# Optimization experiments

Hardware: AMD Instinct MI355X
Metric: run time of the kernel (lower is better)

The kernel has to match this reference:

```python
import jax, jax.numpy as jnp
import numpy as np

MAX_ITERS = 20
TOL = 1e-6
STEP = 1.0
EPS = 1e-7
CLIP = 1e-7


def _normalize(x, axis=-1):
    n = jnp.linalg.norm(x, axis=axis, keepdims=True)
    return x / jnp.maximum(n, 1e-12)


def _safe_acos(x):
    return jnp.arccos(jnp.clip(x, -1.0 + CLIP, 1.0 - CLIP))


def setup_inputs() -> dict:
    key = jax.random.key(0)
    NC, K, N, D = 1000, 8, 32, 128
    X_groups = jax.random.normal(key, (NC, K, N, D), dtype=jnp.float32)
    return {"X_groups": X_groups}


def reference(X_groups):
    # X_groups: (NC, K, N, D)
    NC, K, N, D = X_groups.shape
    X = X_groups.reshape(NC * K, N, D)
    Xn = _normalize(X)                      # (G, N, D) unit vectors
    mu = _normalize(jnp.mean(Xn, axis=1))   # (G, D) init mean

    done = jnp.array(False)
    for _ in range(MAX_ITERS):
        dots = jnp.einsum('gd,gnd->gn', mu, Xn)             # (G, N)
        theta = _safe_acos(dots)
        sin_t = jnp.maximum(jnp.sin(theta), EPS)
        diff = Xn - dots[..., None] * mu[:, None, :]        # (G, N, D)
        log_vecs = (theta / sin_t)[..., None] * diff        # log map
        v = jnp.mean(log_vecs, axis=1)                      # (G, D)
        v_norm = jnp.maximum(jnp.linalg.norm(v, axis=-1, keepdims=True), EPS)
        done = done | (jnp.max(v_norm) < TOL)               # global convergence (as in torch .item() check)
        v_step = STEP * v
        vs_norm = jnp.maximum(jnp.linalg.norm(v_step, axis=-1, keepdims=True), EPS)
        mu_new = jnp.cos(vs_norm) * mu + jnp.sin(vs_norm) * (v_step / vs_norm)  # exp map
        mu_new = _normalize(mu_new)
        mu = jnp.where(done, mu, mu_new)

    # calc_cluster_distance: features (G, N, D) @ means (G, D)
    sims = jnp.einsum('gnd,gd->gn', Xn, mu)
    sims = jnp.clip(sims, -1 + CLIP, 1 - CLIP)
    loss = jnp.mean(jnp.sum(jnp.arccos(sims) ** 2, axis=-1))
    return loss
```

## Files before the change

### kernel.cpp

```cpp
#include <hip/hip_runtime.h>
#include <stdint.h>

#define MAX_ITERS 20
#define EPSV 1e-7f
#define CLIPV 1e-7f
#define PI_F 3.14159265358979f
#define PIO2_F 1.57079632679490f

typedef __attribute__((ext_vector_type(8))) short short8;
typedef __attribute__((ext_vector_type(4))) float f4;

__device__ __forceinline__ f4 mfma_bf16(short8 a, short8 b, f4 c) {
    return __builtin_amdgcn_mfma_f32_16x16x32_bf16(a, b, c, 0, 0, 0);
}

__device__ __forceinline__ float rl(float v, int l) {
    return __int_as_float(__builtin_amdgcn_readlane(__float_as_int(v), l));
}

template <int CTRL>
__device__ __forceinline__ float dpp_add(float v) {
    int p = __builtin_amdgcn_update_dpp(0, __float_as_int(v), CTRL, 0xF, 0xF, true);
    return v + __int_as_float(p);
}
template <int CTRL>
__device__ __forceinline__ float dpp_mov(float v) {
    return __int_as_float(__builtin_amdgcn_update_dpp(0, __float_as_int(v), CTRL, 0xF, 0xF, true));
}

template <int PAT>
__device__ __forceinline__ float swz(float v) {
    return __int_as_float(__builtin_amdgcn_ds_swizzle(__float_as_int(v), PAT));
}

__device__ __forceinline__ float rowsum16(float v) {
    v = dpp_add<0xB1>(v);
    v = dpp_add<0x4E>(v);
    v = dpp_add<0x141>(v);
    v = dpp_add<0x140>(v);
    return v;
}

__device__ __forceinline__ float halfsum_rl(float v, bool hB) {
    v = rowsum16(v);
    float sA = rl(v, 0) + rl(v, 16);
    float sB = rl(v, 32) + rl(v, 48);
    return hB ? sB : sA;
}

__device__ __forceinline__ float halfsum_sw(float v) {
    v = rowsum16(v);
    return v + swz<0x401F>(v);
}

__device__ __forceinline__ float fast_acos(float x) {
    float a = fabsf(x);
    bool big = a > 0.5f;
    float z = big ? 0.5f * (1.0f - a) : x * x;
    float s = big ? sqrtf(z) : x;
    float p = fmaf(z, fmaf(z, fmaf(z, fmaf(z, 4.2163199048e-2f, 2.4181311049e-2f),
                                   4.5470025998e-2f), 7.4953002686e-2f),
                   1.6666752422e-1f);
    float r = fmaf(s * z, p, s);
    float big_val = (x < 0.0f) ? (PI_F - 2.0f * r) : (2.0f * r);
    return big ? big_val : (PIO2_F - r);
}

__device__ __forceinline__ void cvt_hilo(const float* v, short8& hi, short8& lo) {
#pragma unroll
    for (int i = 0; i < 8; ++i) {
        float x = v[i];
        uint32_t u = __float_as_uint(x);
        float hf = __uint_as_float(u & 0xFFFF0000u);
        float lf = x - hf;
        hi[i] = (short)(u >> 16);
        lo[i] = (short)(__float_as_uint(lf) >> 16);
    }
}

#define CHAIN8(cur, acc, B)                                          \
    acc = Grow2[B] * cur;                                            \
    cur = dpp_mov<0xB1>(cur);  acc = fmaf(Grow2[(B)^1],  cur, acc);  \
    cur = dpp_mov<0x4E>(cur);  acc = fmaf(Grow2[(B)^3],  cur, acc);  \
    cur = dpp_mov<0xB1>(cur);  acc = fmaf(Grow2[(B)^2],  cur, acc);  \
    cur = dpp_mov<0x128>(cur); acc = fmaf(Grow2[(B)^10], cur, acc);  \
    cur = dpp_mov<0xB1>(cur);  acc = fmaf(Grow2[(B)^11], cur, acc);  \
    cur = dpp_mov<0x4E>(cur);  acc = fmaf(Grow2[(B)^9],  cur, acc);  \
    cur = dpp_mov<0xB1>(cur);  acc = fmaf(Grow2[(B)^8],  cur, acc);

#define GLOAD_LDS16(srcp, ldsp)                                                   \
    __builtin_amdgcn_global_load_lds(                                             \
        (const __attribute__((address_space(1))) uint32_t*)(srcp),                \
        (__attribute__((address_space(3))) uint32_t*)(ldsp), 16, 0, 0)

#define WAIT_VM(N) do {                                        \
        asm volatile("s_waitcnt vmcnt(" #N ")" ::: "memory");  \
        __builtin_amdgcn_sched_barrier(0);                     \
    } while (0)

__device__ __forceinline__ int gidx(int row, int j) {
    return row * 32 + ((((j >> 2) ^ (row & 7)) << 2) | (j & 3));
}

__global__ void __launch_bounds__(128, 4) karcher(const float* __restrict__ X,
                                                  float* __restrict__ ws,
                                                  int n_groups) {
    __shared__ float lds[2][3072];
    __shared__ float sInv[2][64];
    __shared__ float sPart[4];

    const int lane = threadIdx.x & 63;
    const int wid  = threadIdx.x >> 6;
    const int g0   = blockIdx.x * 4 + wid * 2;
    if (g0 >= n_groups) return;

    const int col  = lane & 15;
    const int quad = lane >> 4;

    float* slot0 = lds[wid];
    float* slot1 = lds[wid] + 1024;
    float* slot2 = lds[wid] + 2048;

    const int rrl = lane >> 3;
    const int g2l = lane & 7;
    auto stage = [&](const float* Xg, int kq, float* slot) {
#pragma unroll
        for (int i = 0; i < 4; ++i) {
            int rr  = i * 8 + rrl;
            int g2s = g2l ^ (rr & 7);
            GLOAD_LDS16(Xg + rr * 128 + kq * 32 + g2s * 4, slot + i * 256);
        }
    };

    const int x0 = col & 7;
    const int b0 = col * 32;
    const int b1 = (col + 16) * 32;
    f4 a00 = {0.f, 0.f, 0.f, 0.f}, a01 = a00, a10 = a00, a11 = a00;
    auto gramq = [&](const float* st) {
        int s0 = ((quad * 2 + 0) ^ x0) * 4;
        int s1 = ((quad * 2 + 1) ^ x0) * 4;
        float r0[8], r1[8];
        *(float4*)(r0)     = *(const float4*)(st + b0 + s0);
        *(float4*)(r0 + 4) = *(const float4*)(st + b0 + s1);
        *(float4*)(r1)     = *(const float4*)(st + b1 + s0);
        *(float4*)(r1 + 4) = *(const float4*)(st + b1 + s1);
        short8 H0, L0, H1, L1;
        cvt_hilo(r0, H0, L0);
        cvt_hilo(r1, H1, L1);
        a00 = mfma_bf16(H0, H0, a00);
        a00 = mfma_bf16(H0, L0, a00);
        a00 = mfma_bf16(L0, H0, a00);
        a01 = mfma_bf16(H0, H1, a01);
        a01 = mfma_bf16(H0, L1, a01);
        a01 = mfma_bf16(L0, H1, a01);
        a10 = mfma_bf16(H1, H0, a10);
        a10 = mfma_bf16(H1, L0, a10);
        a10 = mfma_bf16(L1, H0, a10);
        a11 = mfma_bf16(H1, H1, a11);
        a11 = mfma_bf16(H1, L1, a11);
        a11 = mfma_bf16(L1, H1, a11);
    };
    auto writeG = [&](float* Gs) {
#pragma unroll
        for (int i = 0; i < 4; ++i) {
            int rw = quad * 4 + i;
            Gs[gidx(rw,      col)]      = a00[i];
            Gs[gidx(rw,      col + 16)] = a01[i];
            Gs[gidx(rw + 16, col)]      = a10[i];
            Gs[gidx(rw + 16, col + 16)] = a11[i];
        }
    };

    {
        const float* Xa = X + (size_t)g0 * 4096;
        const float* Xb = X + (size_t)(g0 + 1) * 4096;
        stage(Xa, 0, slot0);
        stage(Xa, 1, slot1);
        WAIT_VM(4);  gramq(slot0);  stage(Xa, 2, slot0);
        WAIT_VM(4);  gramq(slot1);  stage(Xa, 3, slot1);
        WAIT_VM(4);  gramq(slot0);  stage(Xb, 0, slot0);
        WAIT_VM(4);  gramq(slot1);
        writeG(slot2);
        a00 = {0.f, 0.f, 0.f, 0.f}; a01 = a00; a10 = a00; a11 = a00;
        stage(Xb, 1, slot1);
        WAIT_VM(4);  gramq(slot0);  stage(Xb, 2, slot0);
        WAIT_VM(4);  gramq(slot1);  stage(Xb, 3, slot1);
        WAIT_VM(4);  gramq(slot0);
        WAIT_VM(0);  gramq(slot1);
        writeG(slot0);
    }

    const int  half = lane >> 5;
    const bool hB   = half != 0;
    const int  r    = lane & 31;
    const float* Gh = hB ? slot0 : slot2;

    float inv = 1.0f / fmaxf(sqrtf(Gh[gidx(r, r)]), 1e-12f);
    sInv[wid][lane] = inv;
    const float* sI = sInv[wid] + half * 32;

    float Grow2[32];
#pragma unroll
    for (int gg = 0; gg < 32; ++gg) {
        int j = r ^ gg;
        Grow2[gg] = Gh[gidx(r, j)] * (inv * sI[j]);
    }

    float a = 1.0f / 32.0f;
    float ga;
    {
        float s0 = 0, s1 = 0, s2 = 0, s3 = 0;
#pragma unroll
        for (int gg = 0; gg < 8; ++gg) {
            s0 += Grow2[gg];
            s1 += Grow2[gg + 8];
            s2 += Grow2[gg + 16];
            s3 += Grow2[gg + 24];
        }
        ga = ((s0 + s1) + (s2 + s3)) * (1.0f / 32.0f);
        float n2   = halfsum_rl(a * ga, hB);
        float inv0 = 1.0f / fmaxf(sqrtf(n2), 1e-12f);
        a  *= inv0;
        ga *= inv0;
    }

    for (int it = 0; it < MAX_ITERS; ++it) {
        float x  = fminf(fmaxf(ga, -1.0f + CLIPV), 1.0f - CLIPV);
        float th = fast_acos(x);
        float st = fmaxf(sqrtf(fmaxf(1.0f - x * x, 0.0f)), EPSV);
        float w  = __fdividef(th, st);

        float w4  = swz<0x101F>(w);
        float w16 = swz<0x401F>(w);
        float w20 = swz<0x501F>(w);
        float C = halfsum_sw(w * ga);

        float c0 = w,  c1 = w4, c2 = w16, c3 = w20;
        float A0, A1, A2, A3;
        CHAIN8(c0, A0, 0)
        CHAIN8(c1, A1, 4)
        CHAIN8(c2, A2, 16)
        CHAIN8(c3, A3, 20)
        float gw = (A0 + A1) + (A2 + A3);

        float gb   = (gw - C * ga) * (1.0f / 32.0f);
        float beta = (w  - C * a ) * (1.0f / 32.0f);

        float vv = halfsum_rl(beta * gb, hB);
        float vs = fmaxf(sqrtf(fmaxf(vv, 0.0f)), EPSV);
        float cv = __cosf(vs);
        float sv = __fdividef(__sinf(vs), vs);
        a  = fmaf(sv, beta, cv * a);
        ga = fmaf(sv, gb, cv * ga);
        if (__all(vs < 1e-6f)) break;
    }

    float xf = fminf(fmaxf(ga, -1.0f + CLIPV), 1.0f - CLIPV);
    float t  = fast_acos(xf);
    float ls = halfsum_rl(t * t, hB);
    if (r == 0) sPart[wid * 2 + half] = ls;
    __syncthreads();
    if (threadIdx.x == 0)
        ws[blockIdx.x] = (sPart[0] + sPart[1]) + (sPart[2] + sPart[3]);
}

__global__ void __launch_bounds__(256) reduce_partials(const float* __restrict__ ws,
                                                       float* __restrict__ out,
                                                       int n, float scale) {
    __shared__ float sred[4];
    float s = 0.f;
    for (int i = threadIdx.x; i < n; i += 256) s += ws[i];
#pragma unroll
    for (int m = 32; m >= 1; m >>= 1) s += __shfl_xor(s, m, 64);
    const int lane = threadIdx.x & 63, wid = threadIdx.x >> 6;
    if (lane == 0) sred[wid] = s;
    __syncthreads();
    if (threadIdx.x == 0)
        out[0] = ((sred[0] + sred[1]) + (sred[2] + sred[3])) * scale;
}

extern "C" void kernel_launch(void* const* d_in, const int* in_sizes, int n_in,
                              void* d_out, int out_size, void* d_ws, size_t ws_size,
                              hipStream_t stream) {
    const float* X = (const float*)d_in[0];
    float* out = (float*)d_out;
    float* ws = (float*)d_ws;
    int n_groups = in_sizes[0] / (32 * 128);
    int blocks = (n_groups + 3) / 4;
    karcher<<<blocks, 128, 0, stream>>>(X, ws, n_groups);
    reduce_partials<<<1, 256, 0, stream>>>(ws, out, blocks, 1.0f / (float)n_groups);
}
```

Baseline: 213.9 us.

## Map one group per wavefront with finer-grained double-buffered staging

Each wavefront now handles a single group instead of two, and blocks grow to 256 threads with four waves. The Gram staging is restructured into eight smaller 16-column chunks, double-buffered in a 512-float slot per wave, with explicit LDS waits. The aim is more waves in flight to hide global load latency and a smaller per-wave LDS footprint. In exchange, half of each wave's lanes do duplicate work in the per-group iteration, since the two halves of the wave hold the same group, and the reductions now read lanes 0 and 16 only.

```diff
diff --git a/kernel.cpp b/kernel.cpp
--- a/kernel.cpp
+++ b/kernel.cpp
@@ -27,7 +27,6 @@
 __device__ __forceinline__ float dpp_mov(float v) {
     return __int_as_float(__builtin_amdgcn_update_dpp(0, __float_as_int(v), CTRL, 0xF, 0xF, true));
 }
-
 template <int PAT>
 __device__ __forceinline__ float swz(float v) {
     return __int_as_float(__builtin_amdgcn_ds_swizzle(__float_as_int(v), PAT));
@@ -41,16 +40,9 @@
     return v;
 }
 
-__device__ __forceinline__ float halfsum_rl(float v, bool hB) {
+__device__ __forceinline__ float wavesum32(float v) {
     v = rowsum16(v);
-    float sA = rl(v, 0) + rl(v, 16);
-    float sB = rl(v, 32) + rl(v, 48);
-    return hB ? sB : sA;
-}
-
-__device__ __forceinline__ float halfsum_sw(float v) {
-    v = rowsum16(v);
-    return v + swz<0x401F>(v);
+    return rl(v, 0) + rl(v, 16);
 }
 
 __device__ __forceinline__ float fast_acos(float x) {
@@ -97,113 +89,107 @@
         asm volatile("s_waitcnt vmcnt(" #N ")" ::: "memory");  \
         __builtin_amdgcn_sched_barrier(0);                     \
     } while (0)
+#define WAIT_LGKM0() do {                                      \
+        asm volatile("s_waitcnt lgkmcnt(0)" ::: "memory");     \
+        __builtin_amdgcn_sched_barrier(0);                     \
+    } while (0)
 
 __device__ __forceinline__ int gidx(int row, int j) {
     return row * 32 + ((((j >> 2) ^ (row & 7)) << 2) | (j & 3));
 }
 
-__global__ void __launch_bounds__(128, 4) karcher(const float* __restrict__ X,
+__global__ void __launch_bounds__(256, 8) karcher(const float* __restrict__ X,
                                                   float* __restrict__ ws,
                                                   int n_groups) {
-    __shared__ float lds[2][3072];
-    __shared__ float sInv[2][64];
+    __shared__ float lds[4][1024];
+    __shared__ float sInv[4][32];
     __shared__ float sPart[4];
 
     const int lane = threadIdx.x & 63;
     const int wid  = threadIdx.x >> 6;
-    const int g0   = blockIdx.x * 4 + wid * 2;
-    if (g0 >= n_groups) return;
+    const int g    = blockIdx.x * 4 + wid;
+    if (g >= n_groups) return;
 
     const int col  = lane & 15;
     const int quad = lane >> 4;
+    const float* Xg = X + (size_t)g * 4096;
 
     float* slot0 = lds[wid];
-    float* slot1 = lds[wid] + 1024;
-    float* slot2 = lds[wid] + 2048;
-
-    const int rrl = lane >> 3;
-    const int g2l = lane & 7;
-    auto stage = [&](const float* Xg, int kq, float* slot) {
-#pragma unroll
-        for (int i = 0; i < 4; ++i) {
-            int rr  = i * 8 + rrl;
-            int g2s = g2l ^ (rr & 7);
-            GLOAD_LDS16(Xg + rr * 128 + kq * 32 + g2s * 4, slot + i * 256);
+    float* slot1 = lds[wid] + 512;
+
+    const int rrl = lane >> 2;
+    const int gcl = lane & 3;
+    auto stage = [&](int t, float* slot) {
+#pragma unroll
+        for (int i = 0; i < 2; ++i) {
+            int rr = i * 16 + rrl;
+            GLOAD_LDS16(Xg + rr * 128 + t * 16 + gcl * 4, slot + i * 256);
         }
     };
 
-    const int x0 = col & 7;
-    const int b0 = col * 32;
-    const int b1 = (col + 16) * 32;
     f4 a00 = {0.f, 0.f, 0.f, 0.f}, a01 = a00, a10 = a00, a11 = a00;
-    auto gramq = [&](const float* st) {
-        int s0 = ((quad * 2 + 0) ^ x0) * 4;
-        int s1 = ((quad * 2 + 1) ^ x0) * 4;
-        float r0[8], r1[8];
-        *(float4*)(r0)     = *(const float4*)(st + b0 + s0);
-        *(float4*)(r0 + 4) = *(const float4*)(st + b0 + s1);
-        *(float4*)(r1)     = *(const float4*)(st + b1 + s0);
-        *(float4*)(r1 + 4) = *(const float4*)(st + b1 + s1);
-        short8 H0, L0, H1, L1;
-        cvt_hilo(r0, H0, L0);
-        cvt_hilo(r1, H1, L1);
-        a00 = mfma_bf16(H0, H0, a00);
-        a00 = mfma_bf16(H0, L0, a00);
-        a00 = mfma_bf16(L0, H0, a00);
-        a01 = mfma_bf16(H0, H1, a01);
-        a01 = mfma_bf16(H0, L1, a01);
-        a01 = mfma_bf16(L0, H1, a01);
-        a10 = mfma_bf16(H1, H0, a10);
-        a10 = mfma_bf16(H1, L0, a10);
-        a10 = mfma_bf16(L1, H0, a10);
-        a11 = mfma_bf16(H1, H1, a11);
-        a11 = mfma_bf16(H1, L1, a11);
-        a11 = mfma_bf16(L1, H1, a11);
-    };
-    auto writeG = [&](float* Gs) {
-#pragma unroll
-        for (int i = 0; i < 4; ++i) {
-            int rw = quad * 4 + i;
-            Gs[gidx(rw,      col)]      = a00[i];
-            Gs[gidx(rw,      col + 16)] = a01[i];
-            Gs[gidx(rw + 16, col)]      = a10[i];
-            Gs[gidx(rw + 16, col + 16)] = a11[i];
-        }
-    };
-
-    {
-        const float* Xa = X + (size_t)g0 * 4096;
-        const float* Xb = X + (size_t)(g0 + 1) * 4096;
-        stage(Xa, 0, slot0);
-        stage(Xa, 1, slot1);
-        WAIT_VM(4);  gramq(slot0);  stage(Xa, 2, slot0);
-        WAIT_VM(4);  gramq(slot1);  stage(Xa, 3, slot1);
-        WAIT_VM(4);  gramq(slot0);  stage(Xb, 0, slot0);
-        WAIT_VM(4);  gramq(slot1);
-        writeG(slot2);
-        a00 = {0.f, 0.f, 0.f, 0.f}; a01 = a00; a10 = a00; a11 = a00;
-        stage(Xb, 1, slot1);
-        WAIT_VM(4);  gramq(slot0);  stage(Xb, 2, slot0);
-        WAIT_VM(4);  gramq(slot1);  stage(Xb, 3, slot1);
-        WAIT_VM(4);  gramq(slot0);
-        WAIT_VM(0);  gramq(slot1);
-        writeG(slot0);
-    }
-
-    const int  half = lane >> 5;
-    const bool hB   = half != 0;
-    const int  r    = lane & 31;
-    const float* Gh = hB ? slot0 : slot2;
-
-    float inv = 1.0f / fmaxf(sqrtf(Gh[gidx(r, r)]), 1e-12f);
-    sInv[wid][lane] = inv;
-    const float* sI = sInv[wid] + half * 32;
+    float r0[8], r1[8];
+
+#define PHASE(T, WN)                                                        \
+    {                                                                       \
+        WAIT_VM(WN);                                                        \
+        const float* st = ((T) & 1) ? slot1 : slot0;                        \
+        *(float4*)(r0 + 4 * ((T) & 1)) =                                    \
+            *(const float4*)(st + col * 16 + quad * 4);                     \
+        *(float4*)(r1 + 4 * ((T) & 1)) =                                    \
+            *(const float4*)(st + (col + 16) * 16 + quad * 4);              \
+        WAIT_LGKM0();                                                       \
+        if ((T) + 2 < 8) stage((T) + 2, ((T) & 1) ? slot1 : slot0);         \
+        if ((T) & 1) {                                                      \
+            short8 H0, L0, H1, L1;                                          \
+            cvt_hilo(r0, H0, L0);                                           \
+            cvt_hilo(r1, H1, L1);                                           \
+            a00 = mfma_bf16(H0, H0, a00);                                   \
+            a00 = mfma_bf16(H0, L0, a00);                                   \
+            a00 = mfma_bf16(L0, H0, a00);                                   \
+            a01 = mfma_bf16(H0, H1, a01);                                   \
+            a01 = mfma_bf16(H0, L1, a01);                                   \
+            a01 = mfma_bf16(L0, H1, a01);                                   \
+            a10 = mfma_bf16(H1, H0, a10);                                   \
+            a10 = mfma_bf16(H1, L0, a10);                                   \
+            a10 = mfma_bf16(L1, H0, a10);                                   \
+            a11 = mfma_bf16(H1, H1, a11);                                   \
+            a11 = mfma_bf16(H1, L1, a11);                                   \
+            a11 = mfma_bf16(L1, H1, a11);                                   \
+        }                                                                   \
+    }
+
+    stage(0, slot0);
+    stage(1, slot1);
+    PHASE(0, 2)
+    PHASE(1, 2)
+    PHASE(2, 2)
+    PHASE(3, 2)
+    PHASE(4, 2)
+    PHASE(5, 2)
+    PHASE(6, 2)
+    PHASE(7, 0)
+#undef PHASE
+
+    float* Gw = lds[wid];
+#pragma unroll
+    for (int i = 0; i < 4; ++i) {
+        int rw = quad * 4 + i;
+        Gw[gidx(rw,      col)]      = a00[i];
+        Gw[gidx(rw,      col + 16)] = a01[i];
+        Gw[gidx(rw + 16, col)]      = a10[i];
+        Gw[gidx(rw + 16, col + 16)] = a11[i];
+    }
+
+    const int r = lane & 31;
+    float inv = 1.0f / fmaxf(sqrtf(Gw[gidx(r, r)]), 1e-12f);
+    if (lane < 32) sInv[wid][r] = inv;
 
     float Grow2[32];
 #pragma unroll
     for (int gg = 0; gg < 32; ++gg) {
         int j = r ^ gg;
-        Grow2[gg] = Gh[gidx(r, j)] * (inv * sI[j]);
+        Grow2[gg] = Gw[gidx(r, j)] * (inv * sInv[wid][j]);
     }
 
     float a = 1.0f / 32.0f;
@@ -218,7 +204,7 @@
             s3 += Grow2[gg + 24];
         }
         ga = ((s0 + s1) + (s2 + s3)) * (1.0f / 32.0f);
-        float n2   = halfsum_rl(a * ga, hB);
+        float n2   = wavesum32(a * ga);
         float inv0 = 1.0f / fmaxf(sqrtf(n2), 1e-12f);
         a  *= inv0;
         ga *= inv0;
@@ -233,9 +219,9 @@
         float w4  = swz<0x101F>(w);
         float w16 = swz<0x401F>(w);
         float w20 = swz<0x501F>(w);
-        float C = halfsum_sw(w * ga);
-
-        float c0 = w,  c1 = w4, c2 = w16, c3 = w20;
+        float C   = wavesum32(w * ga);
+
+        float c0 = w, c1 = w4, c2 = w16, c3 = w20;
         float A0, A1, A2, A3;
         CHAIN8(c0, A0, 0)
         CHAIN8(c1, A1, 4)
@@ -246,19 +232,19 @@
         float gb   = (gw - C * ga) * (1.0f / 32.0f);
         float beta = (w  - C * a ) * (1.0f / 32.0f);
 
-        float vv = halfsum_rl(beta * gb, hB);
+        float vv = wavesum32(beta * gb);
         float vs = fmaxf(sqrtf(fmaxf(vv, 0.0f)), EPSV);
         float cv = __cosf(vs);
         float sv = __fdividef(__sinf(vs), vs);
         a  = fmaf(sv, beta, cv * a);
         ga = fmaf(sv, gb, cv * ga);
-        if (__all(vs < 1e-6f)) break;
+        if (vs < 1e-6f) break;
     }
 
     float xf = fminf(fmaxf(ga, -1.0f + CLIPV), 1.0f - CLIPV);
     float t  = fast_acos(xf);
-    float ls = halfsum_rl(t * t, hB);
-    if (r == 0) sPart[wid * 2 + half] = ls;
+    float ls = wavesum32(t * t);
+    if (lane == 0) sPart[wid] = ls;
     __syncthreads();
     if (threadIdx.x == 0)
         ws[blockIdx.x] = (sPart[0] + sPart[1]) + (sPart[2] + sPart[3]);
@@ -287,6 +273,6 @@
     float* ws = (float*)d_ws;
     int n_groups = in_sizes[0] / (32 * 128);
     int blocks = (n_groups + 3) / 4;
-    karcher<<<blocks, 128, 0, stream>>>(X, ws, n_groups);
+    karcher<<<blocks, 256, 0, stream>>>(X, ws, n_groups);
     reduce_partials<<<1, 256, 0, stream>>>(ws, out, blocks, 1.0f / (float)n_groups);
 }
```

After: 226.5 us. 1.06x slower.
